# Performance work log

Measured on AMD Instinct MI355X. Metric: run time of the kernel, lower is better.

Reference implementation:

```python
import jax, jax.numpy as jnp
import numpy as np

B, LQ, LK = 4, 2048, 2048
DIM = 1024          # intermediate_dim
H, D = 16, 64       # num_heads, head_dim
AD = H * D          # attn_dim
SCALE = 1.0 / np.sqrt(D).astype(np.float32)


def setup_inputs() -> dict:
    key = jax.random.key(0)
    ks = jax.random.split(key, 12)
    init = lambda k, shape, fan_in: jax.random.normal(k, shape, jnp.float32) / np.sqrt(fan_in).astype(np.float32)
    return {
        "x": jax.random.normal(ks[0], (B, LQ, DIM), jnp.float32),
        "embeds": jax.random.normal(ks[1], (B, LK, DIM), jnp.float32),
        "Wq": init(ks[2], (DIM, AD), DIM), "bq": jnp.zeros((AD,), jnp.float32),
        "Wk": init(ks[3], (DIM, AD), DIM), "bk": jnp.zeros((AD,), jnp.float32),
        "Wv": init(ks[4], (DIM, AD), DIM), "bv": jnp.zeros((AD,), jnp.float32),
        "Wo": init(ks[5], (AD, DIM), AD), "bo": jnp.zeros((DIM,), jnp.float32),
    }


def reference(x, embeds, Wq, bq, Wk, bk, Wv, bv, Wo, bo):
    b, lq, _ = x.shape
    lk = embeds.shape[1]
    # separate QKV projections (cross-attention: K,V from embeds)
    q = (x @ Wq + bq).reshape(b, lq, H, D)
    k = (embeds @ Wk + bk).reshape(b, lk, H, D)
    v = (embeds @ Wv + bv).reshape(b, lk, H, D)
    # scaled dot-product attention; full [b,h,lq,lk] score matrix (as in source)
    scores = jnp.einsum("bqhd,bkhd->bhqk", q, k) * SCALE
    attn = jax.nn.softmax(scores, axis=-1)  # dropout is identity at eval
    ctx = jnp.einsum("bhqk,bkhd->bqhd", attn, v).reshape(b, lq, AD)
    return ctx @ Wo + bo
```

## Files before the change

kernel.cpp:

```cpp
#include <hip/hip_runtime.h>
#include <cstdint>
#include <cstddef>

#define NB   4
#define NLQ  2048
#define NLK  2048
#define NDIM 1024
#define NH   16
#define ND   64
#define NAD  1024

typedef __attribute__((ext_vector_type(8))) short bf16x8;
typedef __attribute__((ext_vector_type(4))) short sh4;
typedef __attribute__((ext_vector_type(4))) float f32x4;

static __device__ __forceinline__ short f2bf(float f) {
    unsigned u = __builtin_bit_cast(unsigned, f);
    u += 0x7fffu + ((u >> 16) & 1u);
    return (short)(u >> 16);
}

#define GLL16(GP, LP) __builtin_amdgcn_global_load_lds( \
    (const __attribute__((address_space(1))) void*)(GP), \
    (__attribute__((address_space(3))) void*)(LP), 16, 0, 0)

template<int CTRL>
static __device__ __forceinline__ float dppmov(float x) {
    return __builtin_bit_cast(float, __builtin_amdgcn_update_dpp(
        __builtin_bit_cast(int, x), __builtin_bit_cast(int, x), CTRL, 0xF, 0xF, true));
}
static __device__ __forceinline__ float rowsum16(float x) {
    x += dppmov<0xB1>(x);
    x += dppmov<0x4E>(x);
    x += dppmov<0x141>(x);
    x += dppmov<0x140>(x);
    return x;
}

__global__ void cvt2(const float* __restrict__ x, const float* __restrict__ e,
                     short* __restrict__ xo, short* __restrict__ eo) {
    const float* in = blockIdx.y ? e : x;
    short* out = blockIdx.y ? eo : xo;
    int i = (blockIdx.x * blockDim.x + threadIdx.x) * 4;
    const float4 v = *(const float4*)(in + i);
    sh4 o;
    o.x = f2bf(v.x); o.y = f2bf(v.y); o.z = f2bf(v.z); o.w = f2bf(v.w);
    *(sh4*)(out + i) = o;
}

__global__ void wtrans4(const float* __restrict__ W0, const float* __restrict__ W1,
                        const float* __restrict__ W2, const float* __restrict__ W3,
                        short* __restrict__ T0, short* __restrict__ T1,
                        short* __restrict__ T2, short* __restrict__ T3) {
    __shared__ float t[32][33];
    const int z = blockIdx.z;
    const float* W = (z == 0) ? W0 : (z == 1) ? W1 : (z == 2) ? W2 : W3;
    short* Wt = (z == 0) ? T0 : (z == 1) ? T1 : (z == 2) ? T2 : T3;
    const int bx = blockIdx.x * 32;
    const int by = blockIdx.y * 32;
    const int tx = threadIdx.x & 31, ty = threadIdx.x >> 5;
    #pragma unroll
    for (int i = 0; i < 32; i += 8)
        t[ty + i][tx] = W[(size_t)(bx + ty + i) * 1024 + by + tx];
    __syncthreads();
    #pragma unroll
    for (int i = 0; i < 32; i += 8)
        Wt[(size_t)(by + ty + i) * 1024 + bx + tx] = f2bf(t[tx][ty + i]);
}

__global__ void vtrans(const short* __restrict__ V, short* __restrict__ Vt) {
    __shared__ __align__(16) short T[64 * 72];
    const int s0 = blockIdx.x * 64;
    const int h = blockIdx.y, b = blockIdx.z;
    const int tid = threadIdx.x;
    const int sr = tid >> 3, c = tid & 7;
    #pragma unroll
    for (int i = 0; i < 2; ++i) {
        const int s = i * 32 + sr;
        const bf16x8 v = *(const bf16x8*)(V + (size_t)(b * NLK + s0 + s) * NAD + h * 64 + c * 8);
        #pragma unroll
        for (int j = 0; j < 8; ++j)
            T[(c * 8 + j) * 72 + s] = v[j];
    }
    __syncthreads();
    #pragma unroll
    for (int i = 0; i < 2; ++i) {
        const int d = i * 32 + sr;
        const bf16x8 o = *(const bf16x8*)&T[d * 72 + c * 8];
        *(bf16x8*)(Vt + ((size_t)((b * NH + h) * 64 + d)) * NLK + s0 + c * 8) = o;
    }
}

__global__ __launch_bounds__(256) void gemm_qkv(const short* __restrict__ Xb,
                                                const short* __restrict__ Eb,
                                                const short* __restrict__ Wqt,
                                                const short* __restrict__ Wkt,
                                                const short* __restrict__ Wvt,
                                                const float* __restrict__ bq,
                                                const float* __restrict__ bk,
                                                const float* __restrict__ bv,
                                                short* __restrict__ Qb,
                                                short* __restrict__ Kf,
                                                short* __restrict__ Vb)
{
    const int N = 1024, K = 1024;
    __shared__ __align__(16) short As[128 * 32];
    __shared__ __align__(16) short Bs[128 * 32];
    const int z = blockIdx.z;
    const short* A    = (z == 0) ? Xb : Eb;
    const short* Wt   = (z == 0) ? Wqt : (z == 1) ? Wkt : Wvt;
    const float* bias = (z == 0) ? bq : (z == 1) ? bk : bv;
    const float scale = (z == 0) ? 0.18033688011112042f : 1.0f;

    const int tid = threadIdx.x, wave = tid >> 6, lane = tid & 63;
    const int quad = lane >> 4, col = lane & 15;
    const int m0 = blockIdx.x * 128, n0 = blockIdx.y * 128;
    const int wm = wave >> 1, wn = wave & 1;

    const f32x4 zero = {0.f, 0.f, 0.f, 0.f};
    f32x4 acc[4][4];
    #pragma unroll
    for (int i = 0; i < 4; ++i)
        #pragma unroll
        for (int j = 0; j < 4; ++j)
            acc[i][j] = zero;

    for (int kt = 0; kt < K / 32; ++kt) {
        __syncthreads();
        #pragma unroll
        for (int i = 0; i < 2; ++i) {
            const int f = (i * 4 + wave) * 512 + lane * 8;
            const int r = f >> 5, c = f & 31;
            GLL16(A  + (size_t)(m0 + r) * K + kt * 32 + c, &As[f]);
            GLL16(Wt + (size_t)(n0 + r) * K + kt * 32 + c, &Bs[f]);
        }
        __syncthreads();
        bf16x8 af[4], bfr[4];
        #pragma unroll
        for (int mt = 0; mt < 4; ++mt)
            af[mt] = *(const bf16x8*)&As[(wm * 64 + mt * 16 + col) * 32 + quad * 8];
        #pragma unroll
        for (int nt = 0; nt < 4; ++nt)
            bfr[nt] = *(const bf16x8*)&Bs[(wn * 64 + nt * 16 + col) * 32 + quad * 8];
        #pragma unroll
        for (int mt = 0; mt < 4; ++mt)
            #pragma unroll
            for (int nt = 0; nt < 4; ++nt)
                acc[mt][nt] = __builtin_amdgcn_mfma_f32_16x16x32_bf16(af[mt], bfr[nt], acc[mt][nt], 0, 0, 0);
    }

    short* outp = (z == 0) ? Qb : (z == 1) ? Kf : Vb;
    #pragma unroll
    for (int mt = 0; mt < 4; ++mt)
        #pragma unroll
        for (int nt = 0; nt < 4; ++nt) {
            const int n = n0 + wn * 64 + nt * 16 + col;
            const float bv_ = bias[n];
            #pragma unroll
            for (int r = 0; r < 4; ++r) {
                const int m = m0 + wm * 64 + mt * 16 + quad * 4 + r;
                outp[(size_t)m * N + n] = f2bf((acc[mt][nt][r] + bv_) * scale);
            }
        }
}

__global__ __launch_bounds__(256) void gemm_out(const short* __restrict__ A,
                                                const short* __restrict__ Wt,
                                                const float* __restrict__ bias,
                                                float* __restrict__ outp)
{
    const int N = 1024, K = 1024;
    __shared__ __align__(16) short As[128 * 32];
    __shared__ __align__(16) short Bs[128 * 32];
    const int tid = threadIdx.x, wave = tid >> 6, lane = tid & 63;
    const int quad = lane >> 4, col = lane & 15;
    const int m0 = blockIdx.x * 128, n0 = blockIdx.y * 128;
    const int wm = wave >> 1, wn = wave & 1;

    const f32x4 zero = {0.f, 0.f, 0.f, 0.f};
    f32x4 acc[4][4];
    #pragma unroll
    for (int i = 0; i < 4; ++i)
        #pragma unroll
        for (int j = 0; j < 4; ++j)
            acc[i][j] = zero;

    for (int kt = 0; kt < K / 32; ++kt) {
        __syncthreads();
        #pragma unroll
        for (int i = 0; i < 2; ++i) {
            const int f = (i * 4 + wave) * 512 + lane * 8;
            const int r = f >> 5, c = f & 31;
            GLL16(A  + (size_t)(m0 + r) * K + kt * 32 + c, &As[f]);
            GLL16(Wt + (size_t)(n0 + r) * K + kt * 32 + c, &Bs[f]);
        }
        __syncthreads();
        bf16x8 af[4], bfr[4];
        #pragma unroll
        for (int mt = 0; mt < 4; ++mt)
            af[mt] = *(const bf16x8*)&As[(wm * 64 + mt * 16 + col) * 32 + quad * 8];
        #pragma unroll
        for (int nt = 0; nt < 4; ++nt)
            bfr[nt] = *(const bf16x8*)&Bs[(wn * 64 + nt * 16 + col) * 32 + quad * 8];
        #pragma unroll
        for (int mt = 0; mt < 4; ++mt)
            #pragma unroll
            for (int nt = 0; nt < 4; ++nt)
                acc[mt][nt] = __builtin_amdgcn_mfma_f32_16x16x32_bf16(af[mt], bfr[nt], acc[mt][nt], 0, 0, 0);
    }

    #pragma unroll
    for (int mt = 0; mt < 4; ++mt)
        #pragma unroll
        for (int nt = 0; nt < 4; ++nt) {
            const int n = n0 + wn * 64 + nt * 16 + col;
            const float bv_ = bias[n];
            #pragma unroll
            for (int r = 0; r < 4; ++r) {
                const int m = m0 + wm * 64 + mt * 16 + quad * 4 + r;
                outp[(size_t)m * N + n] = acc[mt][nt][r] + bv_;
            }
        }
}

__global__ __launch_bounds__(128, 2) void attn_fused4(const short* __restrict__ Q,
                                                      const short* __restrict__ Kb,
                                                      const short* __restrict__ Vt,
                                                      short* __restrict__ ctx)
{
    __shared__ __align__(16) short Ks[64 * 64];
    __shared__ __align__(16) short Vs[64 * 64];
    __shared__ __align__(16) short Ps[2][64 * 72];
    const int tid = threadIdx.x, wave = tid >> 6, lane = tid & 63;
    const int quad = lane >> 4, col = lane & 15;
    const int h = blockIdx.y, b = blockIdx.z;
    const int q0 = blockIdx.x * 128 + wave * 64;

    bf16x8 aq[4][2];
    #pragma unroll
    for (int mt = 0; mt < 4; ++mt) {
        const short* qp = Q + (size_t)(b * NLQ + q0 + mt * 16 + col) * NAD + h * 64 + quad * 8;
        aq[mt][0] = *(const bf16x8*)qp;
        aq[mt][1] = *(const bf16x8*)(qp + 32);
    }

    const f32x4 zero = {0.f, 0.f, 0.f, 0.f};
    f32x4 O[4][4];
    float lp[4][4];
    #pragma unroll
    for (int mt = 0; mt < 4; ++mt) {
        #pragma unroll
        for (int r = 0; r < 4; ++r) lp[mt][r] = 0.f;
        #pragma unroll
        for (int nt = 0; nt < 4; ++nt) O[mt][nt] = zero;
    }

    const int srow = tid >> 3, schunk = tid & 7;
    const short* kbase = Kb + (size_t)b * NLK * NAD + h * 64 + schunk * 8;
    const short* vbase = Vt + (size_t)(b * NH + h) * 64 * NLK + schunk * 8;

    bf16x8 kv[4], vv[4];
    #pragma unroll
    for (int i = 0; i < 4; ++i) {
        const int row = i * 16 + srow;
        kv[i] = *(const bf16x8*)(kbase + (size_t)row * NAD);
        vv[i] = *(const bf16x8*)(vbase + (size_t)row * NLK);
    }

    for (int kt = 0; kt < NLK / 64; ++kt) {
        __syncthreads();
        #pragma unroll
        for (int i = 0; i < 4; ++i) {
            const int row = i * 16 + srow;
            const int c = (schunk ^ (row & 7)) * 8;
            *(bf16x8*)&Ks[row * 64 + c] = kv[i];
            *(bf16x8*)&Vs[row * 64 + c] = vv[i];
        }
        __syncthreads();

        const int nk = (kt + 1) & (NLK / 64 - 1);
        #pragma unroll
        for (int i = 0; i < 4; ++i) {
            const int row = i * 16 + srow;
            kv[i] = *(const bf16x8*)(kbase + (size_t)(nk * 64 + row) * NAD);
            vv[i] = *(const bf16x8*)(vbase + (size_t)row * NLK + nk * 64);
        }

        f32x4 S[4][4];
        #pragma unroll
        for (int mt = 0; mt < 4; ++mt)
            #pragma unroll
            for (int nt = 0; nt < 4; ++nt) S[mt][nt] = zero;
        #pragma unroll
        for (int kk = 0; kk < 2; ++kk)
            #pragma unroll
            for (int nt = 0; nt < 4; ++nt) {
                const int key = nt * 16 + col;
                const bf16x8 bk = *(const bf16x8*)&Ks[key * 64 + (((kk * 4 + quad) ^ (key & 7)) * 8)];
                #pragma unroll
                for (int mt = 0; mt < 4; ++mt)
                    S[mt][nt] = __builtin_amdgcn_mfma_f32_16x16x32_bf16(aq[mt][kk], bk, S[mt][nt], 0, 0, 0);
            }

        #pragma unroll
        for (int mt = 0; mt < 4; ++mt)
            #pragma unroll
            for (int nt = 0; nt < 4; ++nt)
                #pragma unroll
                for (int r = 0; r < 4; ++r) {
                    const unsigned u = __builtin_bit_cast(unsigned,
                        __builtin_amdgcn_exp2f(S[mt][nt][r]));
                    Ps[wave][(mt * 16 + quad * 4 + r) * 72 + nt * 16 + col] = (short)(u >> 16);
                    lp[mt][r] += __builtin_bit_cast(float, u & 0xffff0000u);
                }

        #pragma unroll
        for (int kk = 0; kk < 2; ++kk) {
            bf16x8 pf[4];
            #pragma unroll
            for (int mt = 0; mt < 4; ++mt)
                pf[mt] = *(const bf16x8*)&Ps[wave][(mt * 16 + col) * 72 + kk * 32 + quad * 8];
            #pragma unroll
            for (int nt = 0; nt < 4; ++nt) {
                const int d = nt * 16 + col;
                const bf16x8 bv = *(const bf16x8*)&Vs[d * 64 + (((kk * 4 + quad) ^ (d & 7)) * 8)];
                #pragma unroll
                for (int mt = 0; mt < 4; ++mt)
                    O[mt][nt] = __builtin_amdgcn_mfma_f32_16x16x32_bf16(pf[mt], bv, O[mt][nt], 0, 0, 0);
            }
        }
    }

    #pragma unroll
    for (int mt = 0; mt < 4; ++mt) {
        float linv[4];
        #pragma unroll
        for (int r = 0; r < 4; ++r)
            linv[r] = 1.0f / rowsum16(lp[mt][r]);
        #pragma unroll
        for (int nt = 0; nt < 4; ++nt)
            #pragma unroll
            for (int r = 0; r < 4; ++r) {
                const size_t idx = (size_t)(b * NLQ + q0 + mt * 16 + quad * 4 + r) * NAD
                                 + h * 64 + nt * 16 + col;
                ctx[idx] = f2bf(O[mt][nt][r] * linv[r]);
            }
    }
}

extern "C" void kernel_launch(void* const* d_in, const int* in_sizes, int n_in,
                              void* d_out, int out_size, void* d_ws, size_t ws_size,
                              hipStream_t stream)
{
    (void)in_sizes; (void)n_in; (void)out_size; (void)ws_size;
    const float* x  = (const float*)d_in[0];
    const float* e  = (const float*)d_in[1];
    const float* Wq = (const float*)d_in[2];
    const float* bq = (const float*)d_in[3];
    const float* Wk = (const float*)d_in[4];
    const float* bk = (const float*)d_in[5];
    const float* Wv = (const float*)d_in[6];
    const float* bv = (const float*)d_in[7];
    const float* Wo = (const float*)d_in[8];
    const float* bo = (const float*)d_in[9];
    float* out = (float*)d_out;

    const size_t MQ = (size_t)NB * NLQ;
    short* wsp = (short*)d_ws;
    short* Xb  = wsp;
    short* Eb  = Xb  + MQ * NDIM;
    short* Wqt = Eb  + MQ * NDIM;
    short* Wkt = Wqt + (size_t)NDIM * NAD;
    short* Wvt = Wkt + (size_t)NDIM * NAD;
    short* Wot = Wvt + (size_t)NDIM * NAD;
    short* Qb  = Wot + (size_t)NDIM * NAD;
    short* Kf  = Qb  + MQ * NAD;
    short* Vb  = Kf  + MQ * NAD;
    short* Vtb = Vb  + MQ * NAD;
    short* Cx  = Vtb + MQ * NAD;

    cvt2<<<dim3(8192, 2), 256, 0, stream>>>(x, e, Xb, Eb);
    wtrans4<<<dim3(32, 32, 4), 256, 0, stream>>>(Wq, Wk, Wv, Wo, Wqt, Wkt, Wvt, Wot);

    gemm_qkv<<<dim3(64, 8, 3), 256, 0, stream>>>(Xb, Eb, Wqt, Wkt, Wvt,
                                                 bq, bk, bv, Qb, Kf, Vb);

    vtrans<<<dim3(NLK / 64, NH, NB), 256, 0, stream>>>(Vb, Vtb);

    attn_fused4<<<dim3(NLQ / 128, NH, NB), 128, 0, stream>>>(Qb, Kf, Vtb, Cx);

    gemm_out<<<dim3(64, 8), 256, 0, stream>>>(Cx, Wot, bo, out);
}
```

Baseline: 323.5 us.

## Keep softmax probabilities in registers via transposed S^T MFMA and widen attention blocks

```diff
diff --git a/kernel.cpp b/kernel.cpp
--- a/kernel.cpp
+++ b/kernel.cpp
@@ -13,6 +13,7 @@
 typedef __attribute__((ext_vector_type(8))) short bf16x8;
 typedef __attribute__((ext_vector_type(4))) short sh4;
 typedef __attribute__((ext_vector_type(4))) float f32x4;
+typedef __attribute__((ext_vector_type(4))) int   i32x4;
 
 static __device__ __forceinline__ short f2bf(float f) {
     unsigned u = __builtin_bit_cast(unsigned, f);
@@ -23,19 +24,6 @@
 #define GLL16(GP, LP) __builtin_amdgcn_global_load_lds( \
     (const __attribute__((address_space(1))) void*)(GP), \
     (__attribute__((address_space(3))) void*)(LP), 16, 0, 0)
-
-template<int CTRL>
-static __device__ __forceinline__ float dppmov(float x) {
-    return __builtin_bit_cast(float, __builtin_amdgcn_update_dpp(
-        __builtin_bit_cast(int, x), __builtin_bit_cast(int, x), CTRL, 0xF, 0xF, true));
-}
-static __device__ __forceinline__ float rowsum16(float x) {
-    x += dppmov<0xB1>(x);
-    x += dppmov<0x4E>(x);
-    x += dppmov<0x141>(x);
-    x += dppmov<0x140>(x);
-    return x;
-}
 
 __global__ void cvt2(const float* __restrict__ x, const float* __restrict__ e,
                      short* __restrict__ xo, short* __restrict__ eo) {
@@ -223,18 +211,17 @@
         }
 }
 
-__global__ __launch_bounds__(128, 2) void attn_fused4(const short* __restrict__ Q,
+__global__ __launch_bounds__(256, 2) void attn_fused5(const short* __restrict__ Q,
                                                       const short* __restrict__ Kb,
                                                       const short* __restrict__ Vt,
                                                       short* __restrict__ ctx)
 {
     __shared__ __align__(16) short Ks[64 * 64];
     __shared__ __align__(16) short Vs[64 * 64];
-    __shared__ __align__(16) short Ps[2][64 * 72];
     const int tid = threadIdx.x, wave = tid >> 6, lane = tid & 63;
     const int quad = lane >> 4, col = lane & 15;
     const int h = blockIdx.y, b = blockIdx.z;
-    const int q0 = blockIdx.x * 128 + wave * 64;
+    const int q0 = blockIdx.x * 256 + wave * 64;
 
     bf16x8 aq[4][2];
     #pragma unroll
@@ -246,23 +233,22 @@
 
     const f32x4 zero = {0.f, 0.f, 0.f, 0.f};
     f32x4 O[4][4];
-    float lp[4][4];
+    float lp[4];
     #pragma unroll
     for (int mt = 0; mt < 4; ++mt) {
-        #pragma unroll
-        for (int r = 0; r < 4; ++r) lp[mt][r] = 0.f;
-        #pragma unroll
-        for (int nt = 0; nt < 4; ++nt) O[mt][nt] = zero;
+        lp[mt] = 0.f;
+        #pragma unroll
+        for (int db = 0; db < 4; ++db) O[db][mt] = zero;
     }
 
     const int srow = tid >> 3, schunk = tid & 7;
     const short* kbase = Kb + (size_t)b * NLK * NAD + h * 64 + schunk * 8;
     const short* vbase = Vt + (size_t)(b * NH + h) * 64 * NLK + schunk * 8;
 
-    bf16x8 kv[4], vv[4];
-    #pragma unroll
-    for (int i = 0; i < 4; ++i) {
-        const int row = i * 16 + srow;
+    bf16x8 kv[2], vv[2];
+    #pragma unroll
+    for (int i = 0; i < 2; ++i) {
+        const int row = i * 32 + srow;
         kv[i] = *(const bf16x8*)(kbase + (size_t)row * NAD);
         vv[i] = *(const bf16x8*)(vbase + (size_t)row * NLK);
     }
@@ -270,8 +256,8 @@
     for (int kt = 0; kt < NLK / 64; ++kt) {
         __syncthreads();
         #pragma unroll
-        for (int i = 0; i < 4; ++i) {
-            const int row = i * 16 + srow;
+        for (int i = 0; i < 2; ++i) {
+            const int row = i * 32 + srow;
             const int c = (schunk ^ (row & 7)) * 8;
             *(bf16x8*)&Ks[row * 64 + c] = kv[i];
             *(bf16x8*)&Vs[row * 64 + c] = vv[i];
@@ -280,71 +266,83 @@
 
         const int nk = (kt + 1) & (NLK / 64 - 1);
         #pragma unroll
-        for (int i = 0; i < 4; ++i) {
-            const int row = i * 16 + srow;
+        for (int i = 0; i < 2; ++i) {
+            const int row = i * 32 + srow;
             kv[i] = *(const bf16x8*)(kbase + (size_t)(nk * 64 + row) * NAD);
             vv[i] = *(const bf16x8*)(vbase + (size_t)row * NLK + nk * 64);
         }
 
-        f32x4 S[4][4];
-        #pragma unroll
-        for (int mt = 0; mt < 4; ++mt)
-            #pragma unroll
-            for (int nt = 0; nt < 4; ++nt) S[mt][nt] = zero;
+        bf16x8 kf[2][4];
         #pragma unroll
         for (int kk = 0; kk < 2; ++kk)
             #pragma unroll
             for (int nt = 0; nt < 4; ++nt) {
                 const int key = nt * 16 + col;
-                const bf16x8 bk = *(const bf16x8*)&Ks[key * 64 + (((kk * 4 + quad) ^ (key & 7)) * 8)];
+                kf[kk][nt] = *(const bf16x8*)&Ks[key * 64 + (((kk * 4 + quad) ^ (key & 7)) * 8)];
+            }
+
+        int pk[4][2][4];
+        #pragma unroll
+        for (int mt = 0; mt < 4; ++mt) {
+            f32x4 st[4];
+            #pragma unroll
+            for (int nt = 0; nt < 4; ++nt) st[nt] = zero;
+            #pragma unroll
+            for (int kk = 0; kk < 2; ++kk)
                 #pragma unroll
-                for (int mt = 0; mt < 4; ++mt)
-                    S[mt][nt] = __builtin_amdgcn_mfma_f32_16x16x32_bf16(aq[mt][kk], bk, S[mt][nt], 0, 0, 0);
-            }
-
-        #pragma unroll
-        for (int mt = 0; mt < 4; ++mt)
-            #pragma unroll
-            for (int nt = 0; nt < 4; ++nt)
+                for (int nt = 0; nt < 4; ++nt)
+                    st[nt] = __builtin_amdgcn_mfma_f32_16x16x32_bf16(kf[kk][nt], aq[mt][kk], st[nt], 0, 0, 0);
+            #pragma unroll
+            for (int nt = 0; nt < 4; ++nt) {
+                unsigned u[4];
                 #pragma unroll
                 for (int r = 0; r < 4; ++r) {
-                    const unsigned u = __builtin_bit_cast(unsigned,
-                        __builtin_amdgcn_exp2f(S[mt][nt][r]));
-                    Ps[wave][(mt * 16 + quad * 4 + r) * 72 + nt * 16 + col] = (short)(u >> 16);
-                    lp[mt][r] += __builtin_bit_cast(float, u & 0xffff0000u);
+                    u[r] = __builtin_bit_cast(unsigned, __builtin_amdgcn_exp2f(st[nt][r]));
+                    lp[mt] += __builtin_bit_cast(float, u[r] & 0xffff0000u);
                 }
-
-        #pragma unroll
-        for (int kk = 0; kk < 2; ++kk) {
-            bf16x8 pf[4];
-            #pragma unroll
-            for (int mt = 0; mt < 4; ++mt)
-                pf[mt] = *(const bf16x8*)&Ps[wave][(mt * 16 + col) * 72 + kk * 32 + quad * 8];
-            #pragma unroll
-            for (int nt = 0; nt < 4; ++nt) {
-                const int d = nt * 16 + col;
-                const bf16x8 bv = *(const bf16x8*)&Vs[d * 64 + (((kk * 4 + quad) ^ (d & 7)) * 8)];
+                const int t = nt >> 1, odd = (nt & 1) * 2;
+                pk[mt][t][odd + 0] = (u[0] >> 16) | (u[1] & 0xffff0000u);
+                pk[mt][t][odd + 1] = (u[2] >> 16) | (u[3] & 0xffff0000u);
+            }
+        }
+
+        #pragma unroll
+        for (int t = 0; t < 2; ++t)
+            #pragma unroll
+            for (int db = 0; db < 4; ++db) {
+                const int row = db * 16 + col;
+                const int c0 = t * 32 + quad * 4;
+                const int c1 = t * 32 + 16 + quad * 4;
+                const sh4 lo = *(const sh4*)&Vs[row * 64 + (((c0 >> 3) ^ (row & 7)) * 8 + (c0 & 7))];
+                const sh4 hi = *(const sh4*)&Vs[row * 64 + (((c1 >> 3) ^ (row & 7)) * 8 + (c1 & 7))];
+                bf16x8 va;
                 #pragma unroll
-                for (int mt = 0; mt < 4; ++mt)
-                    O[mt][nt] = __builtin_amdgcn_mfma_f32_16x16x32_bf16(pf[mt], bv, O[mt][nt], 0, 0, 0);
-            }
-        }
+                for (int j = 0; j < 4; ++j) { va[j] = lo[j]; va[j + 4] = hi[j]; }
+                #pragma unroll
+                for (int mt = 0; mt < 4; ++mt) {
+                    const bf16x8 pb = __builtin_bit_cast(bf16x8,
+                        i32x4{pk[mt][t][0], pk[mt][t][1], pk[mt][t][2], pk[mt][t][3]});
+                    O[db][mt] = __builtin_amdgcn_mfma_f32_16x16x32_bf16(va, pb, O[db][mt], 0, 0, 0);
+                }
+            }
     }
 
     #pragma unroll
     for (int mt = 0; mt < 4; ++mt) {
-        float linv[4];
-        #pragma unroll
-        for (int r = 0; r < 4; ++r)
-            linv[r] = 1.0f / rowsum16(lp[mt][r]);
-        #pragma unroll
-        for (int nt = 0; nt < 4; ++nt)
-            #pragma unroll
-            for (int r = 0; r < 4; ++r) {
-                const size_t idx = (size_t)(b * NLQ + q0 + mt * 16 + quad * 4 + r) * NAD
-                                 + h * 64 + nt * 16 + col;
-                ctx[idx] = f2bf(O[mt][nt][r] * linv[r]);
-            }
+        float l = lp[mt];
+        l += __shfl_xor(l, 16, 64);
+        l += __shfl_xor(l, 32, 64);
+        const float linv = 1.0f / l;
+        #pragma unroll
+        for (int db = 0; db < 4; ++db) {
+            sh4 o4;
+            #pragma unroll
+            for (int r = 0; r < 4; ++r)
+                o4[r] = f2bf(O[db][mt][r] * linv);
+            short* cp = ctx + (size_t)(b * NLQ + q0 + mt * 16 + col) * NAD
+                      + h * 64 + db * 16 + quad * 4;
+            *(sh4*)cp = o4;
+        }
     }
 }
 
@@ -387,7 +385,7 @@
 
     vtrans<<<dim3(NLK / 64, NH, NB), 256, 0, stream>>>(Vb, Vtb);
 
-    attn_fused4<<<dim3(NLQ / 128, NH, NB), 128, 0, stream>>>(Qb, Kf, Vtb, Cx);
+    attn_fused5<<<dim3(NLQ / 256, NH, NB), 256, 0, stream>>>(Qb, Kf, Vtb, Cx);
 
     gemm_out<<<dim3(64, 8), 256, 0, stream>>>(Cx, Wot, bo, out);
 }
```

New measurement: 303.6 us. 1.07x faster.
